# Kernel tuning notes

Hardware: AMD Instinct MI355X
Metric: run time of the kernel (lower is better)

## Reference

```python
import jax, jax.numpy as jnp
import numpy as np

NUM_CLASSES = 10000
FEAT_DIM = 1024
BATCH = 4096


def setup_inputs() -> dict:
    key = jax.random.key(0)
    k1, k2 = jax.random.split(key)
    feat = jax.random.normal(k1, (BATCH, FEAT_DIM), dtype=jnp.float32)
    centers = jax.random.normal(k2, (NUM_CLASSES, FEAT_DIM), dtype=jnp.float32)
    return {"feat": feat, "centers": centers}


def reference(feat, centers):
    # logits = -0.5 * ||feat_b - center_c||^2, computed via the GEMM rewrite
    # ||a-b||^2 = ||a||^2 + ||b||^2 - 2 a.b  (same math as broadcast-sub-square-sum,
    # but avoids the [B, C, D] intermediate and uses tensor-core matmul).
    feat_sq = jnp.sum(feat * feat, axis=-1, keepdims=True)          # [B, 1]
    cent_sq = jnp.sum(centers * centers, axis=-1)[None, :]          # [1, C]
    cross = jnp.einsum('bd,cd->bc', feat, centers)                  # [B, C]
    dist = feat_sq + cent_sq - 2.0 * cross                          # [B, C]
    logits = -0.5 * dist
    return logits
```

## Files before the change

kernel.cpp:

```cpp
#include <hip/hip_runtime.h>
#include <hip/hip_bf16.h>
#include <stdint.h>

#define M_DIM 4096
#define N_DIM 10000
#define K_DIM 1024
#define GM (M_DIM / 128)
#define GN ((N_DIM + 127) / 128)
#define SB 16

typedef __attribute__((ext_vector_type(8))) short bf16x8;
typedef __attribute__((ext_vector_type(4))) float f32x4;

__device__ __forceinline__ void async_ld16(const void* g, void* l) {
    __builtin_amdgcn_global_load_lds(
        (const __attribute__((address_space(1))) unsigned int*)g,
        (__attribute__((address_space(3))) unsigned int*)l,
        16, 0, 0);
}

__device__ __forceinline__ unsigned short f2bf(float f) {
    unsigned u = __float_as_uint(f);
    unsigned r = (u + 0x7FFFu + ((u >> 16) & 1u)) >> 16;
    return (unsigned short)r;
}

__global__ __launch_bounds__(256) void prep_rows(
    const float* __restrict__ feat, const float* __restrict__ cent,
    unsigned short* __restrict__ featbf, unsigned short* __restrict__ centbf,
    float* __restrict__ fsq, float* __restrict__ csq)
{
    const int row = blockIdx.x;
    const int t = threadIdx.x;
    const float* in;
    unsigned short* outb;
    float* sqp;
    if (row < M_DIM) {
        in = feat + (size_t)row * K_DIM;
        outb = featbf + (size_t)row * K_DIM;
        sqp = fsq + row;
    } else {
        const int r2 = row - M_DIM;
        in = cent + (size_t)r2 * K_DIM;
        outb = centbf + (size_t)r2 * K_DIM;
        sqp = csq + r2;
    }
    float4 v = ((const float4*)in)[t];
    ushort4 pk;
    pk.x = f2bf(v.x); pk.y = f2bf(v.y); pk.z = f2bf(v.z); pk.w = f2bf(v.w);
    ((ushort4*)outb)[t] = pk;
    float s = v.x * v.x + v.y * v.y + v.z * v.z + v.w * v.w;
    #pragma unroll
    for (int off = 32; off > 0; off >>= 1) s += __shfl_down(s, off, 64);
    __shared__ float ws[4];
    if ((t & 63) == 0) ws[t >> 6] = s;
    __syncthreads();
    if (t == 0) *sqp = ws[0] + ws[1] + ws[2] + ws[3];
}

__global__ __launch_bounds__(256) void gemm_bt(
    const unsigned short* __restrict__ A,
    const unsigned short* __restrict__ B,
    const float* __restrict__ fsq, const float* __restrict__ csq,
    float* __restrict__ out)
{
    __shared__ unsigned short As[128 * 32];
    __shared__ unsigned short Bs[128 * 32];

    const int tid  = threadIdx.x;
    const int lane = tid & 63;
    const int wave = tid >> 6;
    const int wm = wave & 1, wn = wave >> 1;

    const int lin  = blockIdx.x;
    const int band = lin / (SB * GM);
    const int r0   = lin - band * (SB * GM);
    const int bn0  = band * SB;
    int bw = GN - bn0; if (bw > SB) bw = SB;
    const int bm = r0 / bw;
    const int bn = bn0 + (r0 - bm * bw);

    const int arow_base = bm * 128;
    const int brow_base = bn * 128;

    const int srow = tid >> 2;
    const int scol = (tid & 3) * 8;

    const unsigned short* gA0 = A + (size_t)(arow_base + srow) * K_DIM + scol;
    const unsigned short* gA1 = gA0 + (size_t)64 * K_DIM;
    int br0 = brow_base + srow;      if (br0 > N_DIM - 1) br0 = N_DIM - 1;
    int br1 = brow_base + 64 + srow; if (br1 > N_DIM - 1) br1 = N_DIM - 1;
    const unsigned short* gB0 = B + (size_t)br0 * K_DIM + scol;
    const unsigned short* gB1 = B + (size_t)br1 * K_DIM + scol;

    unsigned short* lA0 = As + tid * 8;
    unsigned short* lA1 = As + 2048 + tid * 8;
    unsigned short* lB0 = Bs + tid * 8;
    unsigned short* lB1 = Bs + 2048 + tid * 8;

    f32x4 acc[4][4];
    #pragma unroll
    for (int i = 0; i < 4; i++)
        #pragma unroll
        for (int j = 0; j < 4; j++) {
            f32x4 z = {0.f, 0.f, 0.f, 0.f};
            acc[i][j] = z;
        }

    const int mlane = lane & 15;
    const int quad  = lane >> 4;

    const unsigned short* aptr = As + (wm * 64 + mlane) * 32 + quad * 8;
    const unsigned short* bptr = Bs + (wn * 64 + mlane) * 32 + quad * 8;

    for (int kt = 0; kt < K_DIM / 32; ++kt) {
        async_ld16(gA0, lA0);
        async_ld16(gA1, lA1);
        async_ld16(gB0, lB0);
        async_ld16(gB1, lB1);
        gA0 += 32; gA1 += 32; gB0 += 32; gB1 += 32;
        __syncthreads();

        bf16x8 af[4], bfv[4];
        #pragma unroll
        for (int i = 0; i < 4; i++) {
            af[i]  = *(const bf16x8*)(aptr + i * 16 * 32);
            bfv[i] = *(const bf16x8*)(bptr + i * 16 * 32);
        }
        #pragma unroll
        for (int i = 0; i < 4; i++)
            #pragma unroll
            for (int j = 0; j < 4; j++)
                acc[i][j] = __builtin_amdgcn_mfma_f32_16x16x32_bf16(
                    af[i], bfv[j], acc[i][j], 0, 0, 0);
        __syncthreads();
    }

    const int rbase = arow_base + wm * 64 + quad * 4;
    const int cbase = brow_base + wn * 64 + mlane;
    #pragma unroll
    for (int i = 0; i < 4; i++) {
        float frow[4];
        #pragma unroll
        for (int r = 0; r < 4; r++)
            frow[r] = -0.5f * fsq[rbase + i * 16 + r];
        #pragma unroll
        for (int j = 0; j < 4; j++) {
            int col = cbase + j * 16;
            if (col < N_DIM) {
                float cs = -0.5f * csq[col];
                #pragma unroll
                for (int r = 0; r < 4; r++) {
                    int row = rbase + i * 16 + r;
                    float v = acc[i][j][r] + frow[r] + cs;
                    __builtin_nontemporal_store(v, &out[(size_t)row * N_DIM + col]);
                }
            }
        }
    }
}

extern "C" void kernel_launch(void* const* d_in, const int* in_sizes, int n_in,
                              void* d_out, int out_size, void* d_ws, size_t ws_size,
                              hipStream_t stream) {
    const float* feat = (const float*)d_in[0];
    const float* cent = (const float*)d_in[1];
    float* out = (float*)d_out;

    char* ws = (char*)d_ws;
    unsigned short* featbf = (unsigned short*)ws;
    unsigned short* centbf = (unsigned short*)(ws + 8388608);
    float* fsq = (float*)(ws + 8388608 + 20480000);
    float* csq = (float*)(ws + 8388608 + 20480000 + 16384);

    prep_rows<<<M_DIM + N_DIM, 256, 0, stream>>>(feat, cent, featbf, centbf, fsq, csq);

    gemm_bt<<<GM * GN, 256, 0, stream>>>(featbf, centbf, fsq, csq, out);
}
```

Before: 308.9 us.

## Double-buffer GEMM LDS loads, stage epilogue through LDS, use one wave per row in prep

The GEMM main loop now uses two LDS buffers. The next K-tile's async global-to-LDS loads are issued before the current tile is computed, with explicit vmcnt waits and raw barriers, so load latency overlaps MFMA work. The epilogue writes each wave's results into an LDS scratch tile and reads them back so it can issue 16-byte vectorized nontemporal stores instead of scalar ones. The prep kernel becomes a grid-stride loop with one wave per row and no shared-memory reduction. This doubles LDS use and depends on hand-placed waitcnt and barrier ordering being correct.

```diff
diff --git a/kernel.cpp b/kernel.cpp
--- a/kernel.cpp
+++ b/kernel.cpp
@@ -12,6 +12,11 @@
 typedef __attribute__((ext_vector_type(8))) short bf16x8;
 typedef __attribute__((ext_vector_type(4))) float f32x4;
 
+#define BAR()      asm volatile("s_barrier" ::: "memory")
+#define WAITVM4()  asm volatile("s_waitcnt vmcnt(4)" ::: "memory")
+#define WAITVM0()  asm volatile("s_waitcnt vmcnt(0)" ::: "memory")
+#define WAITLGKM() asm volatile("s_waitcnt lgkmcnt(0)" ::: "memory")
+
 __device__ __forceinline__ void async_ld16(const void* g, void* l) {
     __builtin_amdgcn_global_load_lds(
         (const __attribute__((address_space(1))) unsigned int*)g,
@@ -30,32 +35,36 @@
     unsigned short* __restrict__ featbf, unsigned short* __restrict__ centbf,
     float* __restrict__ fsq, float* __restrict__ csq)
 {
-    const int row = blockIdx.x;
-    const int t = threadIdx.x;
-    const float* in;
-    unsigned short* outb;
-    float* sqp;
-    if (row < M_DIM) {
-        in = feat + (size_t)row * K_DIM;
-        outb = featbf + (size_t)row * K_DIM;
-        sqp = fsq + row;
-    } else {
-        const int r2 = row - M_DIM;
-        in = cent + (size_t)r2 * K_DIM;
-        outb = centbf + (size_t)r2 * K_DIM;
-        sqp = csq + r2;
+    const int wlane = threadIdx.x & 63;
+    const int wid   = blockIdx.x * 4 + (threadIdx.x >> 6);
+    const int nw    = gridDim.x * 4;
+    for (int row = wid; row < M_DIM + N_DIM; row += nw) {
+        const float* in;
+        unsigned short* outb;
+        float* sqp;
+        if (row < M_DIM) {
+            in = feat + (size_t)row * K_DIM;
+            outb = featbf + (size_t)row * K_DIM;
+            sqp = fsq + row;
+        } else {
+            const int r2 = row - M_DIM;
+            in = cent + (size_t)r2 * K_DIM;
+            outb = centbf + (size_t)r2 * K_DIM;
+            sqp = csq + r2;
+        }
+        float s = 0.f;
+        #pragma unroll
+        for (int c = 0; c < 4; c++) {
+            float4 v = ((const float4*)in)[wlane + c * 64];
+            ushort4 pk;
+            pk.x = f2bf(v.x); pk.y = f2bf(v.y); pk.z = f2bf(v.z); pk.w = f2bf(v.w);
+            ((ushort4*)outb)[wlane + c * 64] = pk;
+            s += v.x * v.x + v.y * v.y + v.z * v.z + v.w * v.w;
+        }
+        #pragma unroll
+        for (int off = 32; off > 0; off >>= 1) s += __shfl_down(s, off, 64);
+        if (wlane == 0) *sqp = s;
     }
-    float4 v = ((const float4*)in)[t];
-    ushort4 pk;
-    pk.x = f2bf(v.x); pk.y = f2bf(v.y); pk.z = f2bf(v.z); pk.w = f2bf(v.w);
-    ((ushort4*)outb)[t] = pk;
-    float s = v.x * v.x + v.y * v.y + v.z * v.z + v.w * v.w;
-    #pragma unroll
-    for (int off = 32; off > 0; off >>= 1) s += __shfl_down(s, off, 64);
-    __shared__ float ws[4];
-    if ((t & 63) == 0) ws[t >> 6] = s;
-    __syncthreads();
-    if (t == 0) *sqp = ws[0] + ws[1] + ws[2] + ws[3];
 }
 
 __global__ __launch_bounds__(256) void gemm_bt(
@@ -64,8 +73,7 @@
     const float* __restrict__ fsq, const float* __restrict__ csq,
     float* __restrict__ out)
 {
-    __shared__ unsigned short As[128 * 32];
-    __shared__ unsigned short Bs[128 * 32];
+    __shared__ unsigned short smem[16384];
 
     const int tid  = threadIdx.x;
     const int lane = tid & 63;
@@ -93,11 +101,6 @@
     const unsigned short* gB0 = B + (size_t)br0 * K_DIM + scol;
     const unsigned short* gB1 = B + (size_t)br1 * K_DIM + scol;
 
-    unsigned short* lA0 = As + tid * 8;
-    unsigned short* lA1 = As + 2048 + tid * 8;
-    unsigned short* lB0 = Bs + tid * 8;
-    unsigned short* lB1 = Bs + 2048 + tid * 8;
-
     f32x4 acc[4][4];
     #pragma unroll
     for (int i = 0; i < 4; i++)
@@ -109,55 +112,86 @@
 
     const int mlane = lane & 15;
     const int quad  = lane >> 4;
-
-    const unsigned short* aptr = As + (wm * 64 + mlane) * 32 + quad * 8;
-    const unsigned short* bptr = Bs + (wn * 64 + mlane) * 32 + quad * 8;
-
-    for (int kt = 0; kt < K_DIM / 32; ++kt) {
-        async_ld16(gA0, lA0);
-        async_ld16(gA1, lA1);
-        async_ld16(gB0, lB0);
-        async_ld16(gB1, lB1);
+    const int aoff = (wm * 64 + mlane) * 32 + quad * 8;
+    const int boff = 4096 + (wn * 64 + mlane) * 32 + quad * 8;
+
+    async_ld16(gA0, smem + tid * 8);
+    async_ld16(gA1, smem + 2048 + tid * 8);
+    async_ld16(gB0, smem + 4096 + tid * 8);
+    async_ld16(gB1, smem + 6144 + tid * 8);
+    gA0 += 32; gA1 += 32; gB0 += 32; gB1 += 32;
+
+    #define COMPUTE(bufbase)                                                  \
+        do {                                                                  \
+            const unsigned short* ap = smem + (bufbase) + aoff;               \
+            const unsigned short* bp = smem + (bufbase) + boff;               \
+            bf16x8 af[4], bfv[4];                                             \
+            _Pragma("unroll")                                                 \
+            for (int i = 0; i < 4; i++) {                                     \
+                af[i]  = *(const bf16x8*)(ap + i * 16 * 32);                  \
+                bfv[i] = *(const bf16x8*)(bp + i * 16 * 32);                  \
+            }                                                                 \
+            _Pragma("unroll")                                                 \
+            for (int i = 0; i < 4; i++)                                       \
+                _Pragma("unroll")                                             \
+                for (int j = 0; j < 4; j++)                                   \
+                    acc[i][j] = __builtin_amdgcn_mfma_f32_16x16x32_bf16(      \
+                        af[i], bfv[j], acc[i][j], 0, 0, 0);                   \
+        } while (0)
+
+    for (int kt = 0; kt < K_DIM / 32 - 1; ++kt) {
+        const int buf  = kt & 1;
+        const int nbase = (buf ^ 1) * 8192;
+        async_ld16(gA0, smem + nbase + tid * 8);
+        async_ld16(gA1, smem + nbase + 2048 + tid * 8);
+        async_ld16(gB0, smem + nbase + 4096 + tid * 8);
+        async_ld16(gB1, smem + nbase + 6144 + tid * 8);
         gA0 += 32; gA1 += 32; gB0 += 32; gB1 += 32;
-        __syncthreads();
-
-        bf16x8 af[4], bfv[4];
-        #pragma unroll
-        for (int i = 0; i < 4; i++) {
-            af[i]  = *(const bf16x8*)(aptr + i * 16 * 32);
-            bfv[i] = *(const bf16x8*)(bptr + i * 16 * 32);
-        }
-        #pragma unroll
-        for (int i = 0; i < 4; i++)
-            #pragma unroll
-            for (int j = 0; j < 4; j++)
-                acc[i][j] = __builtin_amdgcn_mfma_f32_16x16x32_bf16(
-                    af[i], bfv[j], acc[i][j], 0, 0, 0);
-        __syncthreads();
+        WAITVM4();
+        BAR();
+        COMPUTE(buf * 8192);
+        BAR();
     }
-
-    const int rbase = arow_base + wm * 64 + quad * 4;
-    const int cbase = brow_base + wn * 64 + mlane;
+    WAITVM0();
+    BAR();
+    COMPUTE(8192);
+    BAR();
+
+    float* W = (float*)smem + wave * 1088;
+    const int rbase0 = arow_base + wm * 64;
+    const int cbase  = brow_base + wn * 64 + mlane;
+    const int rb_col4 = mlane * 4;
+    const int rb_rows = quad;
+    const int gcol4 = brow_base + wn * 64 + rb_col4;
+    const bool colok = gcol4 < N_DIM;
+
     #pragma unroll
     for (int i = 0; i < 4; i++) {
         float frow[4];
         #pragma unroll
         for (int r = 0; r < 4; r++)
-            frow[r] = -0.5f * fsq[rbase + i * 16 + r];
+            frow[r] = -0.5f * fsq[rbase0 + i * 16 + quad * 4 + r];
         #pragma unroll
         for (int j = 0; j < 4; j++) {
             int col = cbase + j * 16;
-            if (col < N_DIM) {
-                float cs = -0.5f * csq[col];
-                #pragma unroll
-                for (int r = 0; r < 4; r++) {
-                    int row = rbase + i * 16 + r;
-                    float v = acc[i][j][r] + frow[r] + cs;
-                    __builtin_nontemporal_store(v, &out[(size_t)row * N_DIM + col]);
-                }
+            float cs = -0.5f * csq[col < N_DIM ? col : (N_DIM - 1)];
+            #pragma unroll
+            for (int r = 0; r < 4; r++)
+                W[(quad * 4 + r) * 68 + j * 16 + mlane] = acc[i][j][r] + frow[r] + cs;
+        }
+        WAITLGKM();
+        #pragma unroll
+        for (int s = 0; s < 4; s++) {
+            int rl = s * 4 + rb_rows;
+            f32x4 v = *(const f32x4*)&W[rl * 68 + rb_col4];
+            if (colok) {
+                int grow = rbase0 + i * 16 + rl;
+                __builtin_nontemporal_store(v, (f32x4*)&out[(size_t)grow * N_DIM + gcol4]);
             }
         }
+        WAITLGKM();
     }
+    #undef COMPUTE
 }
 
 extern "C" void kernel_launch(void* const* d_in, const int* in_sizes, int n_in,
@@ -173,7 +207,7 @@
     float* fsq = (float*)(ws + 8388608 + 20480000);
     float* csq = (float*)(ws + 8388608 + 20480000 + 16384);
 
-    prep_rows<<<M_DIM + N_DIM, 256, 0, stream>>>(feat, cent, featbf, centbf, fsq, csq);
+    prep_rows<<<1024, 256, 0, stream>>>(feat, cent, featbf, centbf, fsq, csq);
 
     gemm_bt<<<GM * GN, 256, 0, stream>>>(featbf, centbf, fsq, csq, out);
 }
```

Result: faster. 296.7 us (-3.9%).
